# Performance work log

Hardware: AMD Instinct MI355X
Metric: run time of the kernel (lower is better)

The kernel has to match this reference:

```python
import jax, jax.numpy as jnp
import numpy as np

SPAN_W = 8      # fixed span width (tokens per span)
HID = 150       # Score hidden dim (hardcoded in source)


def _score_mlp(x, w1, b1, w2, b2, w3, b3):
    # Linear->ReLU->(Dropout=id)->Linear->ReLU->(Dropout=id)->Linear ; out dim 1
    h = jax.nn.relu(x @ w1 + b1)
    h = jax.nn.relu(h @ w2 + b2)
    return h @ w3 + b3


def _make_mlp_params(key, in_dim):
    ks = jax.random.split(key, 6)
    s1 = 1.0 / np.sqrt(in_dim)
    s2 = 1.0 / np.sqrt(HID)
    return (
        jax.random.uniform(ks[0], (in_dim, HID), jnp.float32, -s1, s1),
        jax.random.uniform(ks[1], (HID,), jnp.float32, -s1, s1),
        jax.random.uniform(ks[2], (HID, HID), jnp.float32, -s2, s2),
        jax.random.uniform(ks[3], (HID,), jnp.float32, -s2, s2),
        jax.random.uniform(ks[4], (HID, 1), jnp.float32, -s2, s2),
        jax.random.uniform(ks[5], (1,), jnp.float32, -s2, s2),
    )


def setup_inputs() -> dict:
    key = jax.random.key(0)
    k_emb, k_sp, k_a, k_m, k_p = jax.random.split(key, 5)
    E = 768
    B, T, S = 2, 2048, 96
    encoded_docs = jax.random.normal(k_emb, (B, T, E), jnp.float32)
    span_starts = jnp.sort(
        jax.random.randint(k_sp, (B, S), 0, 2040, dtype=jnp.int64), axis=-1)
    aw1, ab1, aw2, ab2, aw3, ab3 = _make_mlp_params(k_a, E)          # attn Score
    mw1, mb1, mw2, mb2, mw3, mb3 = _make_mlp_params(k_m, 3 * E)      # mention Score
    pw1, pb1, pw2, pb2, pw3, pb3 = _make_mlp_params(k_p, 9 * E)      # pair Score
    return {
        "encoded_docs": encoded_docs, "span_starts": span_starts,
        "aw1": aw1, "ab1": ab1, "aw2": aw2, "ab2": ab2, "aw3": aw3, "ab3": ab3,
        "mw1": mw1, "mb1": mb1, "mw2": mw2, "mb2": mb2, "mw3": mw3, "mb3": mb3,
        "pw1": pw1, "pb1": pb1, "pw2": pw2, "pb2": pb2, "pw3": pw3, "pb3": pb3,
    }


def reference(encoded_docs, span_starts,
              aw1, ab1, aw2, ab2, aw3, ab3,
              mw1, mb1, mw2, mb2, mw3, mb3,
              pw1, pb1, pw2, pb2, pw3, pb3):
    B, T, E = encoded_docs.shape
    S = span_starts.shape[1]

    # --- MentionScore ---
    attns = _score_mlp(encoded_docs, aw1, ab1, aw2, ab2, aw3, ab3)  # [B,T,1]
    starts = span_starts                                              # [B,S]
    ends = starts + (SPAN_W - 1)
    g_start = jnp.take_along_axis(encoded_docs, starts[:, :, None], axis=1)  # [B,S,E]
    g_end = jnp.take_along_axis(encoded_docs, ends[:, :, None], axis=1)      # [B,S,E]
    tok_idx = starts[:, :, None] + jnp.arange(SPAN_W, dtype=starts.dtype)     # [B,S,W]
    flat = tok_idx.reshape(B, S * SPAN_W)
    span_emb = jnp.take_along_axis(encoded_docs, flat[:, :, None], axis=1).reshape(B, S, SPAN_W, E)
    span_attn = jnp.take_along_axis(attns, flat[:, :, None], axis=1).reshape(B, S, SPAN_W, 1)
    g_attn = jnp.sum(span_emb * span_attn, axis=2)                    # [B,S,E]
    g_i = jnp.concatenate([g_start, g_end, g_attn], axis=-1)          # [B,S,3E]
    mention_scores = _score_mlp(g_i, mw1, mb1, mw2, mb2, mw3, mb3)    # [B,S,1]

    # --- PairwiseScore: all pairs (i=span_1, j=span_2) ---
    gi = jnp.broadcast_to(g_i[:, :, None, :], (B, S, S, 3 * E))
    gj = jnp.broadcast_to(g_i[:, None, :, :], (B, S, S, 3 * E))
    pair = jnp.concatenate([gi, gj, gi * gj], axis=-1)                # [B,S,S,9E]
    pair_scores = _score_mlp(pair, pw1, pb1, pw2, pb2, pw3, pb3)      # [B,S,S,1]
    ext = (mention_scores[:, :, None, :] + mention_scores[:, None, :, :] + pair_scores) / 3.0
    return jnp.clip(ext, 0.0, 1.0)
```

## Files before the change

kernel.cpp:

```cpp
#include <hip/hip_runtime.h>

#define EDIM   768
#define E3     2304
#define HIDD   150
#define TT     2048
#define SS     96
#define BB     2

typedef unsigned short u16;
using frag   = __attribute__((ext_vector_type(8))) short;
using f32x4v = __attribute__((ext_vector_type(4))) float;
using u16x8  = __attribute__((ext_vector_type(8))) unsigned short;

__device__ __forceinline__ u16 bf16rn(float f) {
    union { float f; unsigned u; } v; v.f = f;
    unsigned r = v.u + 0x7FFF + ((v.u >> 16) & 1);
    return (u16)(r >> 16);
}
__device__ __forceinline__ float bf16tof(u16 h) {
    union { unsigned u; float f; } v; v.u = ((unsigned)h) << 16;
    return v.f;
}
__device__ __forceinline__ void split2(float f, u16& hi, u16& lo) {
    hi = bf16rn(f); lo = bf16rn(f - bf16tof(hi));
}
__device__ __forceinline__ int swzoff(int row, int qd) {
    return row * 32 + (((qd + (row >> 1)) & 3) << 3);
}
__device__ __forceinline__ void async16(const void* g, void* l) {
    __builtin_amdgcn_global_load_lds(
        (const __attribute__((address_space(1))) void*)g,
        (__attribute__((address_space(3))) void*)l, 16, 0, 0);
}

__global__ __launch_bounds__(256) void k_prep_aw1(
    const float* __restrict__ aw1, u16* __restrict__ W_hi, u16* __restrict__ W_lo)
{
    const int k = blockIdx.x, t = threadIdx.x;
    if (t < 160) {
        float v = (t < HIDD) ? aw1[k * HIDD + t] : 0.f;
        u16 hi, lo; split2(v, hi, lo);
        W_hi[(long)t * EDIM + k] = hi;
        W_lo[(long)t * EDIM + k] = lo;
    }
}

__global__ __launch_bounds__(256) void k_fused1(
    const float* __restrict__ X, const int* __restrict__ spans,
    const u16* __restrict__ AW1t_hi, const u16* __restrict__ AW1t_lo,
    float* __restrict__ AH1,
    const float* __restrict__ pw1, const float* __restrict__ mw1,
    const float* __restrict__ aw2, const float* __restrict__ pw2,
    const float* __restrict__ mw2,
    u16* __restrict__ W12t_hi, u16* __restrict__ W12t_lo,
    u16* __restrict__ AW2t_hi, u16* __restrict__ AW2t_lo,
    u16* __restrict__ PW2t_hi, u16* __restrict__ PW2t_lo,
    u16* __restrict__ MW2t_hi, u16* __restrict__ MW2t_lo)
{
    __shared__ __align__(16) char smem[32768];
    const int id = blockIdx.x;
    const int t  = threadIdx.x;

    if (id < 288) {
        u16* As_hi = (u16*)smem;
        u16* As_lo = (u16*)(smem + 2560);
        u16* Bs_hi = (u16*)(smem + 5120);
        u16* Bs_lo = (u16*)(smem + 17920);

        const int lane = t & 63;
        const int m    = lane & 15;
        const int quad = lane >> 4;
        const int w    = t >> 6;
        const int mt   = (w & 1) * 16;
        const int nb   = (w >> 1) * 80;
        const int rb   = id % 48;
        const int ks   = id / 48;

        const int rr = t >> 3, q = t & 7;
        const int grow = rb * 32 + rr;
        const int bs = grow >> 3, sw = grow & 7;
        const int b  = bs / SS;
        const int tok = spans[bs] + sw;
        const float* arow = X + ((long)b * TT + tok) * EDIM;

        f32x4v acc[5];
        #pragma unroll
        for (int ht = 0; ht < 5; ++ht)
            #pragma unroll
            for (int r = 0; r < 4; ++r) acc[ht][r] = 0.f;

        for (int tt = 0; tt < 4; ++tt) {
            const int kk0 = ks * 128 + tt * 32;
            {
                const float4 xv = *(const float4*)&arow[kk0 + q * 4];
                ushort4 hv, lv;
                split2(xv.x, hv.x, lv.x); split2(xv.y, hv.y, lv.y);
                split2(xv.z, hv.z, lv.z); split2(xv.w, hv.w, lv.w);
                *(ushort4*)&As_hi[rr * 40 + q * 4] = hv;
                *(ushort4*)&As_lo[rr * 40 + q * 4] = lv;
            }
            #pragma unroll
            for (int it = 0; it < 3; ++it) {
                const int v = t + it * 256;
                if (v < 640) {
                    const int h = v >> 2, qq = v & 3;
                    *(uint4*)&Bs_hi[h * 40 + qq * 8] = *(const uint4*)&AW1t_hi[(long)h * EDIM + kk0 + qq * 8];
                    *(uint4*)&Bs_lo[h * 40 + qq * 8] = *(const uint4*)&AW1t_lo[(long)h * EDIM + kk0 + qq * 8];
                }
            }
            __syncthreads();
            const frag ah = *(const frag*)&As_hi[(mt + m) * 40 + quad * 8];
            const frag al = *(const frag*)&As_lo[(mt + m) * 40 + quad * 8];
            #pragma unroll
            for (int ht = 0; ht < 5; ++ht) {
                const frag bh = *(const frag*)&Bs_hi[(nb + ht * 16 + m) * 40 + quad * 8];
                const frag bl = *(const frag*)&Bs_lo[(nb + ht * 16 + m) * 40 + quad * 8];
                acc[ht] = __builtin_amdgcn_mfma_f32_16x16x32_bf16(al, bh, acc[ht], 0, 0, 0);
                acc[ht] = __builtin_amdgcn_mfma_f32_16x16x32_bf16(ah, bl, acc[ht], 0, 0, 0);
                acc[ht] = __builtin_amdgcn_mfma_f32_16x16x32_bf16(ah, bh, acc[ht], 0, 0, 0);
            }
            __syncthreads();
        }
        #pragma unroll
        for (int ht = 0; ht < 5; ++ht) {
            #pragma unroll
            for (int r = 0; r < 4; ++r) {
                const int row = rb * 32 + mt + quad * 4 + r;
                const int col = nb + ht * 16 + m;
                if (col < HIDD) atomicAdd(&AH1[row * 160 + col], acc[ht][r]);
            }
        }
    } else if (id < 1008) {
        float (*tile)[33] = (float(*)[33])smem;
        const int bi = id - 288;
        const int k0 = (bi % 36) * 64;
        const int n0 = (bi / 36) * 32;
        const int seg = n0 / 160;
        const int nloc0 = n0 - seg * 160;
        for (int idx = t; idx < 2048; idx += 256) {
            const int kk = idx >> 5, nn = idx & 31;
            const int nl = nloc0 + nn;
            const int k  = k0 + kk;
            float v = 0.f;
            if (nl < HIDD) {
                if (seg == 0)      v = pw1[(long)k * HIDD + nl];
                else if (seg == 1) v = pw1[(long)(E3 + k) * HIDD + nl];
                else if (seg == 2) v = mw1[(long)k * HIDD + nl];
                else               v = pw1[(long)(2 * E3 + k) * HIDD + nl];
            }
            tile[kk][nn] = v;
        }
        __syncthreads();
        for (int idx = t; idx < 2048; idx += 256) {
            const int nn = idx >> 6, kk = idx & 63;
            u16 hi, lo; split2(tile[kk][nn], hi, lo);
            W12t_hi[(long)(n0 + nn) * E3 + k0 + kk] = hi;
            W12t_lo[(long)(n0 + nn) * E3 + k0 + kk] = lo;
        }
    } else {
        const int r = id - 1008;
        const int k = r % 160;
        const int which = r / 160;
        const float* src = (which == 0) ? aw2 : (which == 1) ? pw2 : mw2;
        u16* dh = (which == 0) ? AW2t_hi : (which == 1) ? PW2t_hi : MW2t_hi;
        u16* dl = (which == 0) ? AW2t_lo : (which == 1) ? PW2t_lo : MW2t_lo;
        if (t < 160) {
            float v = (t < HIDD && k < HIDD) ? src[k * HIDD + t] : 0.f;
            u16 hi, lo; split2(v, hi, lo);
            dh[t * 160 + k] = hi;
            dl[t * 160 + k] = lo;
        }
    }
}

__global__ __launch_bounds__(256) void k_attn2(
    const float* __restrict__ AH1,
    const u16* __restrict__ AW2t_hi, const u16* __restrict__ AW2t_lo,
    const float* __restrict__ ab1, const float* __restrict__ ab2,
    const float* __restrict__ aw3, const float* __restrict__ ab3,
    float* __restrict__ attn_g)
{
    __shared__ __align__(16) u16 As_hi[32 * 40];
    __shared__ __align__(16) u16 As_lo[32 * 40];
    __shared__ __align__(16) u16 Bs_hi[160 * 40];
    __shared__ __align__(16) u16 Bs_lo[160 * 40];
    __shared__ float h1s[32 * 160];
    __shared__ float red[32];

    const int t    = threadIdx.x;
    const int lane = t & 63;
    const int m    = lane & 15;
    const int quad = lane >> 4;
    const int w    = t >> 6;
    const int mt   = (w & 1) * 16;
    const int nb   = (w >> 1) * 80;

    for (int u = t; u < 1280; u += 256) {
        const int row = u / 40, c4 = u - (u / 40) * 40;
        const int c0 = c4 * 4;
        const float4 v = *(const float4*)&AH1[(blockIdx.x * 32 + row) * 160 + c0];
        h1s[row * 160 + c0 + 0] = (c0 + 0 < HIDD) ? fmaxf(v.x + ab1[c0 + 0], 0.f) : 0.f;
        h1s[row * 160 + c0 + 1] = (c0 + 1 < HIDD) ? fmaxf(v.y + ab1[c0 + 1], 0.f) : 0.f;
        h1s[row * 160 + c0 + 2] = (c0 + 2 < HIDD) ? fmaxf(v.z + ab1[c0 + 2], 0.f) : 0.f;
        h1s[row * 160 + c0 + 3] = (c0 + 3 < HIDD) ? fmaxf(v.w + ab1[c0 + 3], 0.f) : 0.f;
    }
    if (t < 32) red[t] = 0.f;
    __syncthreads();

    const int rr = t >> 3, q = t & 7;
    f32x4v acc2[5];
    #pragma unroll
    for (int ht = 0; ht < 5; ++ht)
        #pragma unroll
        for (int r = 0; r < 4; ++r) acc2[ht][r] = 0.f;

    for (int kk = 0; kk < 5; ++kk) {
        {
            const float4 xv = *(const float4*)&h1s[rr * 160 + kk * 32 + q * 4];
            ushort4 hv, lv;
            split2(xv.x, hv.x, lv.x); split2(xv.y, hv.y, lv.y);
            split2(xv.z, hv.z, lv.z); split2(xv.w, hv.w, lv.w);
            *(ushort4*)&As_hi[rr * 40 + q * 4] = hv;
            *(ushort4*)&As_lo[rr * 40 + q * 4] = lv;
        }
        #pragma unroll
        for (int it = 0; it < 3; ++it) {
            const int v = t + it * 256;
            if (v < 640) {
                const int h = v >> 2, qq = v & 3;
                *(uint4*)&Bs_hi[h * 40 + qq * 8] = *(const uint4*)&AW2t_hi[h * 160 + kk * 32 + qq * 8];
                *(uint4*)&Bs_lo[h * 40 + qq * 8] = *(const uint4*)&AW2t_lo[h * 160 + kk * 32 + qq * 8];
            }
        }
        __syncthreads();
        const frag ah = *(const frag*)&As_hi[(mt + m) * 40 + quad * 8];
        const frag al = *(const frag*)&As_lo[(mt + m) * 40 + quad * 8];
        #pragma unroll
        for (int ht = 0; ht < 5; ++ht) {
            const frag bh = *(const frag*)&Bs_hi[(nb + ht * 16 + m) * 40 + quad * 8];
            const frag bl = *(const frag*)&Bs_lo[(nb + ht * 16 + m) * 40 + quad * 8];
            acc2[ht] = __builtin_amdgcn_mfma_f32_16x16x32_bf16(al, bh, acc2[ht], 0, 0, 0);
            acc2[ht] = __builtin_amdgcn_mfma_f32_16x16x32_bf16(ah, bl, acc2[ht], 0, 0, 0);
            acc2[ht] = __builtin_amdgcn_mfma_f32_16x16x32_bf16(ah, bh, acc2[ht], 0, 0, 0);
        }
        __syncthreads();
    }

    float s[4] = {0.f, 0.f, 0.f, 0.f};
    #pragma unroll
    for (int ht = 0; ht < 5; ++ht) {
        const int col = nb + ht * 16 + m;
        if (col < HIDD) {
            const float w3 = aw3[col];
            #pragma unroll
            for (int r = 0; r < 4; ++r)
                s[r] += fmaxf(acc2[ht][r] + ab2[col], 0.f) * w3;
        }
    }
    #pragma unroll
    for (int r = 0; r < 4; ++r) {
        for (int off = 8; off > 0; off >>= 1) s[r] += __shfl_down(s[r], off, 16);
    }
    if (m == 0) {
        #pragma unroll
        for (int r = 0; r < 4; ++r) atomicAdd(&red[mt + quad * 4 + r], s[r]);
    }
    __syncthreads();
    if (t < 32) attn_g[blockIdx.x * 32 + t] = red[t] + ab3[0];
}

__global__ __launch_bounds__(256) void k_span_g(
    const float* __restrict__ X, const int* __restrict__ spans,
    const float* __restrict__ attn_g, float* __restrict__ G_ws,
    u16* __restrict__ Gs_hi, u16* __restrict__ Gs_lo)
{
    __shared__ float a8[8];
    const int t  = threadIdx.x;
    const int bs = blockIdx.x;
    const int b  = bs / SS;
    const int start = spans[bs];
    const float* xb = X + ((long)b * TT + start) * EDIM;
    float* Gp = G_ws + (long)bs * E3;
    u16* Gh = Gs_hi + (long)bs * E3;
    u16* Gl = Gs_lo + (long)bs * E3;
    if (t < 8) a8[t] = attn_g[bs * 8 + t];
    __syncthreads();

    for (int e = t; e < EDIM; e += 256) {
        const float gs = xb[e];
        const float ge = xb[7 * EDIM + e];
        float ga = 0.f;
        #pragma unroll
        for (int w = 0; w < 8; ++w) ga += xb[w * EDIM + e] * a8[w];
        Gp[e] = gs; Gp[EDIM + e] = ge; Gp[2 * EDIM + e] = ga;
        u16 hi, lo;
        split2(gs, hi, lo); Gh[e] = hi;            Gl[e] = lo;
        split2(ge, hi, lo); Gh[EDIM + e] = hi;     Gl[EDIM + e] = lo;
        split2(ga, hi, lo); Gh[2 * EDIM + e] = hi; Gl[2 * EDIM + e] = lo;
    }
}

__global__ __launch_bounds__(256) void k_heavy(
    const float* __restrict__ G_ws,
    const u16* __restrict__ Gs_hi, const u16* __restrict__ Gs_lo,
    const u16* __restrict__ W12t_hi, const u16* __restrict__ W12t_lo,
    const u16* __restrict__ PCt_hi, const u16* __restrict__ PCt_lo,
    float* __restrict__ H1parts, float* __restrict__ UVM)
{
    __shared__ __align__(16) char smem[48128];
    const int id = blockIdx.x;
    const int t  = threadIdx.x;
    const int lane = t & 63;
    const int m    = lane & 15;
    const int quad = lane >> 4;
    const int w    = t >> 6;

    if (id < 576) {
        float* gis  = (float*)smem;
        float* gjst = (float*)(smem + 3072);
        u16* As_hi  = (u16*)(smem + 15360);
        u16* As_lo  = (u16*)(smem + 21504);
        u16* Bs_hi  = (u16*)(smem + 27648);
        u16* Bs_lo  = (u16*)(smem + 37888);

        const int ks = id % 3;
        const int i  = (id / 3) % SS;
        const int b  = id / 288;
        const int ksbase = ks * 768;
        const int jt0 = i >> 4;
        const int ntiles = 6 - jt0;
        const int j0 = jt0 * 16;
        const int R  = 96 - j0;
        const int nI = R >> 3;

        const int hb   = (w & 1) * 80;
        const int apar = w >> 1;
        const int Bl_h = lane >> 2;
        const int Bl_c = lane & 3;
        const int gj_r = lane >> 3;
        const int gj_c = lane & 7;

        const float* Gi = G_ws + (long)(b * SS + i) * E3 + ksbase;
        for (int e = t; e < 768; e += 256) gis[e] = Gi[e];

        f32x4v acc[3][5];
        #pragma unroll
        for (int jt = 0; jt < 3; ++jt)
            #pragma unroll
            for (int ht = 0; ht < 5; ++ht)
                #pragma unroll
                for (int r = 0; r < 4; ++r) acc[jt][ht][r] = 0.f;

        for (int tt = 0; tt < 24; ++tt) {
            const int kk0 = ksbase + tt * 32;
            for (int q2 = w; q2 < 10; q2 += 4) {
                const int h  = q2 * 16 + Bl_h;
                const int qd = (Bl_c - (h >> 1)) & 3;
                const long so = (long)h * E3 + kk0 + qd * 8;
                async16(&PCt_hi[so], &Bs_hi[q2 * 512]);
                async16(&PCt_lo[so], &Bs_lo[q2 * 512]);
            }
            for (int g2 = w; g2 < nI; g2 += 4) {
                const int row = j0 + g2 * 8 + gj_r;
                async16(&G_ws[(long)(b * SS + row) * E3 + kk0 + gj_c * 4],
                        &gjst[g2 * 256]);
            }
            __syncthreads();

            for (int u = t; u < R * 4; u += 256) {
                const int rr = u >> 2, qd = u & 3;
                const float4 g0 = *(const float4*)&gjst[rr * 32 + qd * 8];
                const float4 g1 = *(const float4*)&gjst[rr * 32 + qd * 8 + 4];
                const int kl = tt * 32 + qd * 8;
                u16x8 hv, lv; u16 h, l;
                split2(g0.x * gis[kl + 0], h, l); hv[0] = h; lv[0] = l;
                split2(g0.y * gis[kl + 1], h, l); hv[1] = h; lv[1] = l;
                split2(g0.z * gis[kl + 2], h, l); hv[2] = h; lv[2] = l;
                split2(g0.w * gis[kl + 3], h, l); hv[3] = h; lv[3] = l;
                split2(g1.x * gis[kl + 4], h, l); hv[4] = h; lv[4] = l;
                split2(g1.y * gis[kl + 5], h, l); hv[5] = h; lv[5] = l;
                split2(g1.z * gis[kl + 6], h, l); hv[6] = h; lv[6] = l;
                split2(g1.w * gis[kl + 7], h, l); hv[7] = h; lv[7] = l;
                const int o = swzoff(rr, qd);
                *(u16x8*)&As_hi[o] = hv;
                *(u16x8*)&As_lo[o] = lv;
            }
            __syncthreads();

            frag ah[3], al[3];
            #pragma unroll
            for (int u = 0; u < 3; ++u) {
                const int a = apar + 2 * u;
                if (a < ntiles) {
                    const int o = swzoff(a * 16 + m, quad);
                    ah[u] = *(const frag*)&As_hi[o];
                    al[u] = *(const frag*)&As_lo[o];
                }
            }
            #pragma unroll
            for (int ht = 0; ht < 5; ++ht) {
                const int o = swzoff(hb + ht * 16 + m, quad);
                const frag bh = *(const frag*)&Bs_hi[o];
                const frag bl = *(const frag*)&Bs_lo[o];
                #pragma unroll
                for (int u = 0; u < 3; ++u) {
                    if (apar + 2 * u < ntiles) {
                        acc[u][ht] = __builtin_amdgcn_mfma_f32_16x16x32_bf16(al[u], bh, acc[u][ht], 0, 0, 0);
                        acc[u][ht] = __builtin_amdgcn_mfma_f32_16x16x32_bf16(ah[u], bl, acc[u][ht], 0, 0, 0);
                        acc[u][ht] = __builtin_amdgcn_mfma_f32_16x16x32_bf16(ah[u], bh, acc[u][ht], 0, 0, 0);
                    }
                }
            }
            __syncthreads();
        }

        float* dst = H1parts + (long)ks * ((long)BB * SS * SS * 160);
        #pragma unroll
        for (int u = 0; u < 3; ++u) {
            const int a = apar + 2 * u;
            if (a < ntiles) {
                #pragma unroll
                for (int ht = 0; ht < 5; ++ht) {
                    #pragma unroll
                    for (int r = 0; r < 4; ++r) {
                        const int j = (jt0 + a) * 16 + quad * 4 + r;
                        const int h = hb + ht * 16 + m;
                        dst[((long)(b * SS + i) * SS + j) * 160 + h] = acc[u][ht][r];
                    }
                }
            }
        }
    } else {
        u16* As_hi = (u16*)smem;
        u16* As_lo = (u16*)(smem + 5120);
        u16* Bs_hi = (u16*)(smem + 10240);
        u16* Bs_lo = (u16*)(smem + 23040);

        const int u0 = id - 576;
        const int mb = u0 % 3;
        const int nb = (u0 / 3) % 3;
        const int kz = u0 / 9;
        const int mhalf = (w & 1) * 32;
        const int nbase = (w >> 1) * 80;
        const int arr = t >> 2, aq = t & 3;

        f32x4v acc[2][5];
        #pragma unroll
        for (int i = 0; i < 2; ++i)
            #pragma unroll
            for (int j = 0; j < 5; ++j)
                #pragma unroll
                for (int r = 0; r < 4; ++r) acc[i][j][r] = 0.f;

        for (int tt = 0; tt < 6; ++tt) {
            const int kk0 = kz * 192 + tt * 32;
            *(uint4*)&As_hi[arr * 40 + aq * 8] = *(const uint4*)&Gs_hi[(long)(mb * 64 + arr) * E3 + kk0 + aq * 8];
            *(uint4*)&As_lo[arr * 40 + aq * 8] = *(const uint4*)&Gs_lo[(long)(mb * 64 + arr) * E3 + kk0 + aq * 8];
            #pragma unroll
            for (int it = 0; it < 3; ++it) {
                const int v = t + it * 256;
                if (v < 640) {
                    const int h = v >> 2, qq = v & 3;
                    *(uint4*)&Bs_hi[h * 40 + qq * 8] = *(const uint4*)&W12t_hi[(long)(nb * 160 + h) * E3 + kk0 + qq * 8];
                    *(uint4*)&Bs_lo[h * 40 + qq * 8] = *(const uint4*)&W12t_lo[(long)(nb * 160 + h) * E3 + kk0 + qq * 8];
                }
            }
            __syncthreads();
            frag ah[2], al[2];
            #pragma unroll
            for (int mt = 0; mt < 2; ++mt) {
                ah[mt] = *(const frag*)&As_hi[(mhalf + mt * 16 + m) * 40 + quad * 8];
                al[mt] = *(const frag*)&As_lo[(mhalf + mt * 16 + m) * 40 + quad * 8];
            }
            #pragma unroll
            for (int ht = 0; ht < 5; ++ht) {
                const frag bh = *(const frag*)&Bs_hi[(nbase + ht * 16 + m) * 40 + quad * 8];
                const frag bl = *(const frag*)&Bs_lo[(nbase + ht * 16 + m) * 40 + quad * 8];
                #pragma unroll
                for (int mt = 0; mt < 2; ++mt) {
                    acc[mt][ht] = __builtin_amdgcn_mfma_f32_16x16x32_bf16(al[mt], bh, acc[mt][ht], 0, 0, 0);
                    acc[mt][ht] = __builtin_amdgcn_mfma_f32_16x16x32_bf16(ah[mt], bl, acc[mt][ht], 0, 0, 0);
                    acc[mt][ht] = __builtin_amdgcn_mfma_f32_16x16x32_bf16(ah[mt], bh, acc[mt][ht], 0, 0, 0);
                }
            }
            __syncthreads();
        }
        float* dst = UVM + (long)nb * (192 * 160);
        #pragma unroll
        for (int mt = 0; mt < 2; ++mt) {
            #pragma unroll
            for (int ht = 0; ht < 5; ++ht) {
                #pragma unroll
                for (int r = 0; r < 4; ++r) {
                    const int row = mb * 64 + mhalf + mt * 16 + quad * 4 + r;
                    const int c   = nbase + ht * 16 + m;
                    atomicAdd(&dst[row * 160 + c], acc[mt][ht][r]);
                }
            }
        }
    }
}

__global__ __launch_bounds__(256) void k_pair2(
    const float* __restrict__ H1parts,
    const float* __restrict__ U_ws, const float* __restrict__ V_ws,
    const float* __restrict__ pb1, const float* __restrict__ m_ws,
    const u16* __restrict__ PW2t_hi, const u16* __restrict__ PW2t_lo,
    const float* __restrict__ pb2, const float* __restrict__ pw3,
    const float* __restrict__ pb3,
    float* __restrict__ out)
{
    __shared__ __align__(16) u16 As_hi[32 * 168];
    __shared__ __align__(16) u16 As_lo[32 * 168];
    __shared__ __align__(16) u16 Bs_hi[160 * 40];
    __shared__ __align__(16) u16 Bs_lo[160 * 40];
    __shared__ float uv[160];
    __shared__ float red[32];

    const long partsz = (long)BB * SS * SS * 160;
    const int t  = threadIdx.x;
    const int js = blockIdx.x;
    const int bi = blockIdx.y;
    const int b  = bi / SS;
    const int ii = bi - b * SS;
    const int jb0 = js * 32;

    if (t < 160) uv[t] = U_ws[bi * 160 + t] + ((t < HIDD) ? pb1[t] : 0.f);
    if (t < 32) red[t] = 0.f;
    __syncthreads();

    for (int u = t; u < 32 * 40; u += 256) {
        const int jl = u / 40, hq = u - (u / 40) * 40;
        const int j  = jb0 + jl;
        const int h0 = hq * 4;
        const int mn = ii < j ? ii : j;
        const int mx = ii < j ? j : ii;
        const long idx = (((long)b * SS + mn) * SS + mx) * 160 + h0;
        const float4 vv = *(const float4*)&V_ws[(b * SS + j) * 160 + h0];
        const float4 a0 = *(const float4*)&H1parts[idx];
        const float4 a1 = *(const float4*)&H1parts[partsz + idx];
        const float4 a2 = *(const float4*)&H1parts[2 * partsz + idx];
        const float p0 = fmaxf(a0.x + a1.x + a2.x + vv.x + uv[h0 + 0], 0.f);
        const float p1 = fmaxf(a0.y + a1.y + a2.y + vv.y + uv[h0 + 1], 0.f);
        const float p2 = fmaxf(a0.z + a1.z + a2.z + vv.z + uv[h0 + 2], 0.f);
        const float p3 = fmaxf(a0.w + a1.w + a2.w + vv.w + uv[h0 + 3], 0.f);
        ushort4 hv, lv;
        split2(p0, hv.x, lv.x); split2(p1, hv.y, lv.y);
        split2(p2, hv.z, lv.z); split2(p3, hv.w, lv.w);
        *(ushort4*)&As_hi[jl * 168 + h0] = hv;
        *(ushort4*)&As_lo[jl * 168 + h0] = lv;
    }
    __syncthreads();

    const int lane = t & 63;
    const int m    = lane & 15;
    const int quad = lane >> 4;
    const int w    = t >> 6;
    const int jt   = w >> 1;
    const int nbs  = (w & 1) * 80;

    f32x4v acc[5];
    #pragma unroll
    for (int ht = 0; ht < 5; ++ht)
        #pragma unroll
        for (int r = 0; r < 4; ++r) acc[ht][r] = 0.f;

    for (int kk = 0; kk < 5; ++kk) {
        #pragma unroll
        for (int it = 0; it < 3; ++it) {
            const int v = t + it * 256;
            if (v < 640) {
                const int n = v >> 2, qq = v & 3;
                *(uint4*)&Bs_hi[n * 40 + qq * 8] = *(const uint4*)&PW2t_hi[n * 160 + kk * 32 + qq * 8];
                *(uint4*)&Bs_lo[n * 40 + qq * 8] = *(const uint4*)&PW2t_lo[n * 160 + kk * 32 + qq * 8];
            }
        }
        __syncthreads();
        const frag ah = *(const frag*)&As_hi[(jt * 16 + m) * 168 + kk * 32 + quad * 8];
        const frag al = *(const frag*)&As_lo[(jt * 16 + m) * 168 + kk * 32 + quad * 8];
        #pragma unroll
        for (int ht = 0; ht < 5; ++ht) {
            const frag bh = *(const frag*)&Bs_hi[(nbs + ht * 16 + m) * 40 + quad * 8];
            const frag bl = *(const frag*)&Bs_lo[(nbs + ht * 16 + m) * 40 + quad * 8];
            acc[ht] = __builtin_amdgcn_mfma_f32_16x16x32_bf16(al, bh, acc[ht], 0, 0, 0);
            acc[ht] = __builtin_amdgcn_mfma_f32_16x16x32_bf16(ah, bl, acc[ht], 0, 0, 0);
            acc[ht] = __builtin_amdgcn_mfma_f32_16x16x32_bf16(ah, bh, acc[ht], 0, 0, 0);
        }
        __syncthreads();
    }

    float s[4] = {0.f, 0.f, 0.f, 0.f};
    #pragma unroll
    for (int ht = 0; ht < 5; ++ht) {
        const int col = nbs + ht * 16 + m;
        if (col < HIDD) {
            const float w3 = pw3[col];
            const float b2 = pb2[col];
            #pragma unroll
            for (int r = 0; r < 4; ++r)
                s[r] += fmaxf(acc[ht][r] + b2, 0.f) * w3;
        }
    }
    #pragma unroll
    for (int r = 0; r < 4; ++r)
        for (int off = 8; off > 0; off >>= 1)
            s[r] += __shfl_down(s[r], off, 16);
    if (m == 0) {
        #pragma unroll
        for (int r = 0; r < 4; ++r)
            atomicAdd(&red[jt * 16 + quad * 4 + r], s[r]);
    }
    __syncthreads();

    if (t < 32) {
        const int j = jb0 + t;
        const float sc = red[t] + pb3[0];
        const float v = (m_ws[bi] + m_ws[b * SS + j] + sc) * (1.f / 3.f);
        out[(long)bi * SS + j] = fminf(fmaxf(v, 0.f), 1.f);
    }
}

extern "C" void kernel_launch(void* const* d_in, const int* in_sizes, int n_in,
                              void* d_out, int out_size, void* d_ws, size_t ws_size,
                              hipStream_t stream)
{
    const float* X     = (const float*)d_in[0];
    const int*   spans = (const int*)  d_in[1];
    const float* aw1 = (const float*)d_in[2];
    const float* ab1 = (const float*)d_in[3];
    const float* aw2 = (const float*)d_in[4];
    const float* ab2 = (const float*)d_in[5];
    const float* aw3 = (const float*)d_in[6];
    const float* ab3 = (const float*)d_in[7];
    const float* mw1 = (const float*)d_in[8];
    const float* mb1 = (const float*)d_in[9];
    const float* mw2 = (const float*)d_in[10];
    const float* mb2 = (const float*)d_in[11];
    const float* mw3 = (const float*)d_in[12];
    const float* mb3 = (const float*)d_in[13];
    const float* pw1 = (const float*)d_in[14];
    const float* pb1 = (const float*)d_in[15];
    const float* pw2 = (const float*)d_in[16];
    const float* pb2 = (const float*)d_in[17];
    const float* pw3 = (const float*)d_in[18];
    const float* pb3 = (const float*)d_in[19];
    float* out = (float*)d_out;

    char* p = (char*)d_ws;
    float* attn_g  = (float*)p;  p += 6144;
    float* G_ws    = (float*)p;  p += (long)442368 * 4;
    u16*   Gs_hi   = (u16*)p;    p += (long)442368 * 2;
    u16*   Gs_lo   = (u16*)p;    p += (long)442368 * 2;
    float* UVM     = (float*)p;  p += (long)3 * 192 * 160 * 4;
    float* AH1     = (float*)p;  p += (long)1536 * 160 * 4;
    float* m_ws    = (float*)p;  p += 1024;
    u16*   W12t_hi = (u16*)p;    p += (long)640 * E3 * 2;
    u16*   W12t_lo = (u16*)p;    p += (long)640 * E3 * 2;
    u16*   AW1t_hi = (u16*)p;    p += (long)160 * EDIM * 2;
    u16*   AW1t_lo = (u16*)p;    p += (long)160 * EDIM * 2;
    u16*   AW2t_hi = (u16*)p;    p += 160 * 160 * 2;
    u16*   AW2t_lo = (u16*)p;    p += 160 * 160 * 2;
    u16*   PW2t_hi = (u16*)p;    p += 160 * 160 * 2;
    u16*   PW2t_lo = (u16*)p;    p += 160 * 160 * 2;
    u16*   MW2t_hi = (u16*)p;    p += 160 * 160 * 2;
    u16*   MW2t_lo = (u16*)p;    p += 160 * 160 * 2;
    float* H1parts = (float*)p;

    float* U_ws = UVM;
    float* V_ws = UVM + 192 * 160;
    float* M_ws = UVM + 2 * 192 * 160;
    const u16* PCt_hi = W12t_hi + (long)480 * E3;
    const u16* PCt_lo = W12t_lo + (long)480 * E3;

    hipMemsetAsync(UVM, 0, ((size_t)3 * 192 * 160 + (size_t)1536 * 160) * sizeof(float), stream);

    k_prep_aw1<<<dim3(EDIM), 256, 0, stream>>>(aw1, AW1t_hi, AW1t_lo);

    k_fused1<<<dim3(1488), 256, 0, stream>>>(X, spans, AW1t_hi, AW1t_lo, AH1,
                                             pw1, mw1, aw2, pw2, mw2,
                                             W12t_hi, W12t_lo, AW2t_hi, AW2t_lo,
                                             PW2t_hi, PW2t_lo, MW2t_hi, MW2t_lo);

    k_attn2<<<dim3(48), 256, 0, stream>>>(AH1, AW2t_hi, AW2t_lo, ab1, ab2, aw3, ab3, attn_g);
    k_span_g<<<dim3(BB * SS), 256, 0, stream>>>(X, spans, attn_g, G_ws, Gs_hi, Gs_lo);

    k_heavy<<<dim3(684), 256, 0, stream>>>(G_ws, Gs_hi, Gs_lo, W12t_hi, W12t_lo,
                                           PCt_hi, PCt_lo, H1parts, UVM);

    k_attn2<<<dim3(6), 256, 0, stream>>>(M_ws, MW2t_hi, MW2t_lo, mb1, mb2, mw3, mb3, m_ws);

    k_pair2<<<dim3(3, BB * SS), 256, 0, stream>>>(
        H1parts, U_ws, V_ws, pb1, m_ws, PW2t_hi, PW2t_lo, pb2, pw3, pb3, out);
}
```

Baseline: 213.9 us.

## Merge small dependent kernels using in-kernel atomic flags and split-K partial buffers

Fuses the attention-MLP second layer with span embedding gathering, and the mention-score MLP with the pairwise final stage, into single launches. Inside each merged launch, consumer blocks spin on a global atomic counter until the producer blocks signal completion. The first-layer attention GEMM now writes split-K partials to separate buffers instead of using atomicAdd, and the consumer sums them, which also shrinks the memset. This removes launch gaps and atomic contention, but spin-waiting assumes the producer blocks are scheduled before or alongside the waiters, and the merged kernels use more shared memory.

```diff
diff --git a/kernel.cpp b/kernel.cpp
--- a/kernel.cpp
+++ b/kernel.cpp
@@ -31,6 +31,17 @@
     __builtin_amdgcn_global_load_lds(
         (const __attribute__((address_space(1))) void*)g,
         (__attribute__((address_space(3))) void*)l, 16, 0, 0);
+}
+__device__ __forceinline__ void signal_done(int* flag) {
+    __syncthreads();
+    if (threadIdx.x == 0)
+        __hip_atomic_fetch_add(flag, 1, __ATOMIC_RELEASE, __HIP_MEMORY_SCOPE_AGENT);
+}
+__device__ __forceinline__ void wait_for(int* flag, int target) {
+    if (threadIdx.x == 0) {
+        while (__hip_atomic_load(flag, __ATOMIC_ACQUIRE, __HIP_MEMORY_SCOPE_AGENT) < target) {}
+    }
+    __syncthreads();
 }
 
 __global__ __launch_bounds__(256) void k_prep_aw1(
@@ -48,7 +59,7 @@
 __global__ __launch_bounds__(256) void k_fused1(
     const float* __restrict__ X, const int* __restrict__ spans,
     const u16* __restrict__ AW1t_hi, const u16* __restrict__ AW1t_lo,
-    float* __restrict__ AH1,
+    float* __restrict__ AH1parts,
     const float* __restrict__ pw1, const float* __restrict__ mw1,
     const float* __restrict__ aw2, const float* __restrict__ pw2,
     const float* __restrict__ mw2,
@@ -121,13 +132,14 @@
             }
             __syncthreads();
         }
+        float* dst = AH1parts + (long)ks * (1536 * 160);
         #pragma unroll
         for (int ht = 0; ht < 5; ++ht) {
             #pragma unroll
             for (int r = 0; r < 4; ++r) {
                 const int row = rb * 32 + mt + quad * 4 + r;
                 const int col = nb + ht * 16 + m;
-                if (col < HIDD) atomicAdd(&AH1[row * 160 + col], acc[ht][r]);
+                dst[row * 160 + col] = acc[ht][r];
             }
         }
     } else if (id < 1008) {
@@ -173,130 +185,143 @@
     }
 }
 
-__global__ __launch_bounds__(256) void k_attn2(
-    const float* __restrict__ AH1,
+__global__ __launch_bounds__(256) void k_attn2span(
+    const float* __restrict__ X, const int* __restrict__ spans,
+    const float* __restrict__ AH1parts,
     const u16* __restrict__ AW2t_hi, const u16* __restrict__ AW2t_lo,
     const float* __restrict__ ab1, const float* __restrict__ ab2,
     const float* __restrict__ aw3, const float* __restrict__ ab3,
-    float* __restrict__ attn_g)
+    float* __restrict__ attn_g, float* __restrict__ G_ws,
+    u16* __restrict__ Gs_hi, u16* __restrict__ Gs_lo,
+    int* __restrict__ flag)
 {
-    __shared__ __align__(16) u16 As_hi[32 * 40];
-    __shared__ __align__(16) u16 As_lo[32 * 40];
-    __shared__ __align__(16) u16 Bs_hi[160 * 40];
-    __shared__ __align__(16) u16 Bs_lo[160 * 40];
-    __shared__ float h1s[32 * 160];
-    __shared__ float red[32];
-
-    const int t    = threadIdx.x;
-    const int lane = t & 63;
-    const int m    = lane & 15;
-    const int quad = lane >> 4;
-    const int w    = t >> 6;
-    const int mt   = (w & 1) * 16;
-    const int nb   = (w >> 1) * 80;
-
-    for (int u = t; u < 1280; u += 256) {
-        const int row = u / 40, c4 = u - (u / 40) * 40;
-        const int c0 = c4 * 4;
-        const float4 v = *(const float4*)&AH1[(blockIdx.x * 32 + row) * 160 + c0];
-        h1s[row * 160 + c0 + 0] = (c0 + 0 < HIDD) ? fmaxf(v.x + ab1[c0 + 0], 0.f) : 0.f;
-        h1s[row * 160 + c0 + 1] = (c0 + 1 < HIDD) ? fmaxf(v.y + ab1[c0 + 1], 0.f) : 0.f;
-        h1s[row * 160 + c0 + 2] = (c0 + 2 < HIDD) ? fmaxf(v.z + ab1[c0 + 2], 0.f) : 0.f;
-        h1s[row * 160 + c0 + 3] = (c0 + 3 < HIDD) ? fmaxf(v.w + ab1[c0 + 3], 0.f) : 0.f;
-    }
-    if (t < 32) red[t] = 0.f;
-    __syncthreads();
-
-    const int rr = t >> 3, q = t & 7;
-    f32x4v acc2[5];
-    #pragma unroll
-    for (int ht = 0; ht < 5; ++ht)
-        #pragma unroll
-        for (int r = 0; r < 4; ++r) acc2[ht][r] = 0.f;
-
-    for (int kk = 0; kk < 5; ++kk) {
-        {
-            const float4 xv = *(const float4*)&h1s[rr * 160 + kk * 32 + q * 4];
-            ushort4 hv, lv;
-            split2(xv.x, hv.x, lv.x); split2(xv.y, hv.y, lv.y);
-            split2(xv.z, hv.z, lv.z); split2(xv.w, hv.w, lv.w);
-            *(ushort4*)&As_hi[rr * 40 + q * 4] = hv;
-            *(ushort4*)&As_lo[rr * 40 + q * 4] = lv;
-        }
-        #pragma unroll
-        for (int it = 0; it < 3; ++it) {
-            const int v = t + it * 256;
-            if (v < 640) {
-                const int h = v >> 2, qq = v & 3;
-                *(uint4*)&Bs_hi[h * 40 + qq * 8] = *(const uint4*)&AW2t_hi[h * 160 + kk * 32 + qq * 8];
-                *(uint4*)&Bs_lo[h * 40 + qq * 8] = *(const uint4*)&AW2t_lo[h * 160 + kk * 32 + qq * 8];
-            }
-        }
+    __shared__ __align__(16) char smem[51328];
+    const int id = blockIdx.x;
+    const int t  = threadIdx.x;
+
+    if (id < 48) {
+        u16* As_hi = (u16*)smem;
+        u16* As_lo = (u16*)(smem + 2560);
+        u16* Bs_hi = (u16*)(smem + 5120);
+        u16* Bs_lo = (u16*)(smem + 17920);
+        float* h1s = (float*)(smem + 30720);
+        float* red = (float*)(smem + 51200);
+
+        const int lane = t & 63;
+        const int m    = lane & 15;
+        const int quad = lane >> 4;
+        const int w    = t >> 6;
+        const int mt   = (w & 1) * 16;
+        const int nb   = (w >> 1) * 80;
+
+        for (int u = t; u < 1280; u += 256) {
+            const int row = u / 40, c4 = u - (u / 40) * 40;
+            const int c0 = c4 * 4;
+            const long off = (long)(id * 32 + row) * 160 + c0;
+            float4 s = *(const float4*)&AH1parts[off];
+            #pragma unroll
+            for (int pp = 1; pp < 6; ++pp) {
+                const float4 v = *(const float4*)&AH1parts[(long)pp * 245760 + off];
+                s.x += v.x; s.y += v.y; s.z += v.z; s.w += v.w;
+            }
+            h1s[row * 160 + c0 + 0] = (c0 + 0 < HIDD) ? fmaxf(s.x + ab1[c0 + 0], 0.f) : 0.f;
+            h1s[row * 160 + c0 + 1] = (c0 + 1 < HIDD) ? fmaxf(s.y + ab1[c0 + 1], 0.f) : 0.f;
+            h1s[row * 160 + c0 + 2] = (c0 + 2 < HIDD) ? fmaxf(s.z + ab1[c0 + 2], 0.f) : 0.f;
+            h1s[row * 160 + c0 + 3] = (c0 + 3 < HIDD) ? fmaxf(s.w + ab1[c0 + 3], 0.f) : 0.f;
+        }
+        if (t < 32) red[t] = 0.f;
         __syncthreads();
-        const frag ah = *(const frag*)&As_hi[(mt + m) * 40 + quad * 8];
-        const frag al = *(const frag*)&As_lo[(mt + m) * 40 + quad * 8];
+
+        const int rr = t >> 3, q = t & 7;
+        f32x4v acc2[5];
+        #pragma unroll
+        for (int ht = 0; ht < 5; ++ht)
+            #pragma unroll
+            for (int r = 0; r < 4; ++r) acc2[ht][r] = 0.f;
+
+        for (int kk = 0; kk < 5; ++kk) {
+            {
+                const float4 xv = *(const float4*)&h1s[rr * 160 + kk * 32 + q * 4];
+                ushort4 hv, lv;
+                split2(xv.x, hv.x, lv.x); split2(xv.y, hv.y, lv.y);
+                split2(xv.z, hv.z, lv.z); split2(xv.w, hv.w, lv.w);
+                *(ushort4*)&As_hi[rr * 40 + q * 4] = hv;
+                *(ushort4*)&As_lo[rr * 40 + q * 4] = lv;
+            }
+            #pragma unroll
+            for (int it = 0; it < 3; ++it) {
+                const int v = t + it * 256;
+                if (v < 640) {
+                    const int h = v >> 2, qq = v & 3;
+                    *(uint4*)&Bs_hi[h * 40 + qq * 8] = *(const uint4*)&AW2t_hi[h * 160 + kk * 32 + qq * 8];
+                    *(uint4*)&Bs_lo[h * 40 + qq * 8] = *(const uint4*)&AW2t_lo[h * 160 + kk * 32 + qq * 8];
+                }
+            }
+            __syncthreads();
+            const frag ah = *(const frag*)&As_hi[(mt + m) * 40 + quad * 8];
+            const frag al = *(const frag*)&As_lo[(mt + m) * 40 + quad * 8];
+            #pragma unroll
+            for (int ht = 0; ht < 5; ++ht) {
+                const frag bh = *(const frag*)&Bs_hi[(nb + ht * 16 + m) * 40 + quad * 8];
+                const frag bl = *(const frag*)&Bs_lo[(nb + ht * 16 + m) * 40 + quad * 8];
+                acc2[ht] = __builtin_amdgcn_mfma_f32_16x16x32_bf16(al, bh, acc2[ht], 0, 0, 0);
+                acc2[ht] = __builtin_amdgcn_mfma_f32_16x16x32_bf16(ah, bl, acc2[ht], 0, 0, 0);
+                acc2[ht] = __builtin_amdgcn_mfma_f32_16x16x32_bf16(ah, bh, acc2[ht], 0, 0, 0);
+            }
+            __syncthreads();
+        }
+
+        float s[4] = {0.f, 0.f, 0.f, 0.f};
         #pragma unroll
         for (int ht = 0; ht < 5; ++ht) {
-            const frag bh = *(const frag*)&Bs_hi[(nb + ht * 16 + m) * 40 + quad * 8];
-            const frag bl = *(const frag*)&Bs_lo[(nb + ht * 16 + m) * 40 + quad * 8];
-            acc2[ht] = __builtin_amdgcn_mfma_f32_16x16x32_bf16(al, bh, acc2[ht], 0, 0, 0);
-            acc2[ht] = __builtin_amdgcn_mfma_f32_16x16x32_bf16(ah, bl, acc2[ht], 0, 0, 0);
-            acc2[ht] = __builtin_amdgcn_mfma_f32_16x16x32_bf16(ah, bh, acc2[ht], 0, 0, 0);
+            const int col = nb + ht * 16 + m;
+            if (col < HIDD) {
+                const float w3 = aw3[col];
+                #pragma unroll
+                for (int r = 0; r < 4; ++r)
+                    s[r] += fmaxf(acc2[ht][r] + ab2[col], 0.f) * w3;
+            }
+        }
+        #pragma unroll
+        for (int r = 0; r < 4; ++r) {
+            for (int off = 8; off > 0; off >>= 1) s[r] += __shfl_down(s[r], off, 16);
+        }
+        if (m == 0) {
+            #pragma unroll
+            for (int r = 0; r < 4; ++r) atomicAdd(&red[mt + quad * 4 + r], s[r]);
         }
         __syncthreads();
-    }
-
-    float s[4] = {0.f, 0.f, 0.f, 0.f};
-    #pragma unroll
-    for (int ht = 0; ht < 5; ++ht) {
-        const int col = nb + ht * 16 + m;
-        if (col < HIDD) {
-            const float w3 = aw3[col];
-            #pragma unroll
-            for (int r = 0; r < 4; ++r)
-                s[r] += fmaxf(acc2[ht][r] + ab2[col], 0.f) * w3;
-        }
-    }
-    #pragma unroll
-    for (int r = 0; r < 4; ++r) {
-        for (int off = 8; off > 0; off >>= 1) s[r] += __shfl_down(s[r], off, 16);
-    }
-    if (m == 0) {
-        #pragma unroll
-        for (int r = 0; r < 4; ++r) atomicAdd(&red[mt + quad * 4 + r], s[r]);
-    }
-    __syncthreads();
-    if (t < 32) attn_g[blockIdx.x * 32 + t] = red[t] + ab3[0];
-}
-
-__global__ __launch_bounds__(256) void k_span_g(
-    const float* __restrict__ X, const int* __restrict__ spans,
-    const float* __restrict__ attn_g, float* __restrict__ G_ws,
-    u16* __restrict__ Gs_hi, u16* __restrict__ Gs_lo)
-{
-    __shared__ float a8[8];
-    const int t  = threadIdx.x;
-    const int bs = blockIdx.x;
-    const int b  = bs / SS;
-    const int start = spans[bs];
-    const float* xb = X + ((long)b * TT + start) * EDIM;
-    float* Gp = G_ws + (long)bs * E3;
-    u16* Gh = Gs_hi + (long)bs * E3;
-    u16* Gl = Gs_lo + (long)bs * E3;
-    if (t < 8) a8[t] = attn_g[bs * 8 + t];
-    __syncthreads();
-
-    for (int e = t; e < EDIM; e += 256) {
-        const float gs = xb[e];
-        const float ge = xb[7 * EDIM + e];
-        float ga = 0.f;
-        #pragma unroll
-        for (int w = 0; w < 8; ++w) ga += xb[w * EDIM + e] * a8[w];
-        Gp[e] = gs; Gp[EDIM + e] = ge; Gp[2 * EDIM + e] = ga;
-        u16 hi, lo;
-        split2(gs, hi, lo); Gh[e] = hi;            Gl[e] = lo;
-        split2(ge, hi, lo); Gh[EDIM + e] = hi;     Gl[EDIM + e] = lo;
-        split2(ga, hi, lo); Gh[2 * EDIM + e] = hi; Gl[2 * EDIM + e] = lo;
+        if (t < 32) attn_g[id * 32 + t] = red[t] + ab3[0];
+        signal_done(flag);
+    } else {
+        float* a8 = (float*)smem;
+        const int bs = id - 48;
+        const int b  = bs / SS;
+        const int start = spans[bs];
+        const float* xb = X + ((long)b * TT + start) * EDIM;
+        float* Gp = G_ws + (long)bs * E3;
+        u16* Gh = Gs_hi + (long)bs * E3;
+        u16* Gl = Gs_lo + (long)bs * E3;
+
+        for (int e = t; e < EDIM; e += 256) {
+            const float gs = xb[e];
+            const float ge = xb[7 * EDIM + e];
+            Gp[e] = gs; Gp[EDIM + e] = ge;
+            u16 hi, lo;
+            split2(gs, hi, lo); Gh[e] = hi;        Gl[e] = lo;
+            split2(ge, hi, lo); Gh[EDIM + e] = hi; Gl[EDIM + e] = lo;
+        }
+        wait_for(flag, 48);
+        if (t < 8) a8[t] = attn_g[bs * 8 + t];
+        __syncthreads();
+        for (int e = t; e < EDIM; e += 256) {
+            float ga = 0.f;
+            #pragma unroll
+            for (int w = 0; w < 8; ++w) ga += xb[w * EDIM + e] * a8[w];
+            Gp[2 * EDIM + e] = ga;
+            u16 hi, lo; split2(ga, hi, lo);
+            Gh[2 * EDIM + e] = hi; Gl[2 * EDIM + e] = lo;
+        }
     }
 }
 
@@ -501,122 +526,218 @@
     }
 }
 
-__global__ __launch_bounds__(256) void k_pair2(
+__global__ __launch_bounds__(256) void k_final(
     const float* __restrict__ H1parts,
     const float* __restrict__ U_ws, const float* __restrict__ V_ws,
-    const float* __restrict__ pb1, const float* __restrict__ m_ws,
+    const float* __restrict__ M_ws,
+    const float* __restrict__ pb1, float* __restrict__ m_ws,
     const u16* __restrict__ PW2t_hi, const u16* __restrict__ PW2t_lo,
+    const u16* __restrict__ MW2t_hi, const u16* __restrict__ MW2t_lo,
+    const float* __restrict__ mb1, const float* __restrict__ mb2,
+    const float* __restrict__ mw3, const float* __restrict__ mb3,
     const float* __restrict__ pb2, const float* __restrict__ pw3,
     const float* __restrict__ pb3,
+    int* __restrict__ flag,
     float* __restrict__ out)
 {
-    __shared__ __align__(16) u16 As_hi[32 * 168];
-    __shared__ __align__(16) u16 As_lo[32 * 168];
-    __shared__ __align__(16) u16 Bs_hi[160 * 40];
-    __shared__ __align__(16) u16 Bs_lo[160 * 40];
-    __shared__ float uv[160];
-    __shared__ float red[32];
-
-    const long partsz = (long)BB * SS * SS * 160;
+    __shared__ __align__(16) char smem[51328];
+    const int id = blockIdx.x;
     const int t  = threadIdx.x;
-    const int js = blockIdx.x;
-    const int bi = blockIdx.y;
-    const int b  = bi / SS;
-    const int ii = bi - b * SS;
-    const int jb0 = js * 32;
-
-    if (t < 160) uv[t] = U_ws[bi * 160 + t] + ((t < HIDD) ? pb1[t] : 0.f);
-    if (t < 32) red[t] = 0.f;
-    __syncthreads();
-
-    for (int u = t; u < 32 * 40; u += 256) {
-        const int jl = u / 40, hq = u - (u / 40) * 40;
-        const int j  = jb0 + jl;
-        const int h0 = hq * 4;
-        const int mn = ii < j ? ii : j;
-        const int mx = ii < j ? j : ii;
-        const long idx = (((long)b * SS + mn) * SS + mx) * 160 + h0;
-        const float4 vv = *(const float4*)&V_ws[(b * SS + j) * 160 + h0];
-        const float4 a0 = *(const float4*)&H1parts[idx];
-        const float4 a1 = *(const float4*)&H1parts[partsz + idx];
-        const float4 a2 = *(const float4*)&H1parts[2 * partsz + idx];
-        const float p0 = fmaxf(a0.x + a1.x + a2.x + vv.x + uv[h0 + 0], 0.f);
-        const float p1 = fmaxf(a0.y + a1.y + a2.y + vv.y + uv[h0 + 1], 0.f);
-        const float p2 = fmaxf(a0.z + a1.z + a2.z + vv.z + uv[h0 + 2], 0.f);
-        const float p3 = fmaxf(a0.w + a1.w + a2.w + vv.w + uv[h0 + 3], 0.f);
-        ushort4 hv, lv;
-        split2(p0, hv.x, lv.x); split2(p1, hv.y, lv.y);
-        split2(p2, hv.z, lv.z); split2(p3, hv.w, lv.w);
-        *(ushort4*)&As_hi[jl * 168 + h0] = hv;
-        *(ushort4*)&As_lo[jl * 168 + h0] = lv;
-    }
-    __syncthreads();
-
     const int lane = t & 63;
     const int m    = lane & 15;
     const int quad = lane >> 4;
     const int w    = t >> 6;
-    const int jt   = w >> 1;
-    const int nbs  = (w & 1) * 80;
-
-    f32x4v acc[5];
-    #pragma unroll
-    for (int ht = 0; ht < 5; ++ht)
-        #pragma unroll
-        for (int r = 0; r < 4; ++r) acc[ht][r] = 0.f;
-
-    for (int kk = 0; kk < 5; ++kk) {
-        #pragma unroll
-        for (int it = 0; it < 3; ++it) {
-            const int v = t + it * 256;
-            if (v < 640) {
-                const int n = v >> 2, qq = v & 3;
-                *(uint4*)&Bs_hi[n * 40 + qq * 8] = *(const uint4*)&PW2t_hi[n * 160 + kk * 32 + qq * 8];
-                *(uint4*)&Bs_lo[n * 40 + qq * 8] = *(const uint4*)&PW2t_lo[n * 160 + kk * 32 + qq * 8];
-            }
-        }
+
+    if (id < 6) {
+        u16* As_hi = (u16*)smem;
+        u16* As_lo = (u16*)(smem + 2560);
+        u16* Bs_hi = (u16*)(smem + 5120);
+        u16* Bs_lo = (u16*)(smem + 17920);
+        float* h1s = (float*)(smem + 30720);
+        float* red = (float*)(smem + 51200);
+
+        const int mt = (w & 1) * 16;
+        const int nb = (w >> 1) * 80;
+
+        for (int u = t; u < 1280; u += 256) {
+            const int row = u / 40, c4 = u - (u / 40) * 40;
+            const int c0 = c4 * 4;
+            const float4 v = *(const float4*)&M_ws[(id * 32 + row) * 160 + c0];
+            h1s[row * 160 + c0 + 0] = (c0 + 0 < HIDD) ? fmaxf(v.x + mb1[c0 + 0], 0.f) : 0.f;
+            h1s[row * 160 + c0 + 1] = (c0 + 1 < HIDD) ? fmaxf(v.y + mb1[c0 + 1], 0.f) : 0.f;
+            h1s[row * 160 + c0 + 2] = (c0 + 2 < HIDD) ? fmaxf(v.z + mb1[c0 + 2], 0.f) : 0.f;
+            h1s[row * 160 + c0 + 3] = (c0 + 3 < HIDD) ? fmaxf(v.w + mb1[c0 + 3], 0.f) : 0.f;
+        }
+        if (t < 32) red[t] = 0.f;
         __syncthreads();
-        const frag ah = *(const frag*)&As_hi[(jt * 16 + m) * 168 + kk * 32 + quad * 8];
-        const frag al = *(const frag*)&As_lo[(jt * 16 + m) * 168 + kk * 32 + quad * 8];
+
+        const int rr = t >> 3, q = t & 7;
+        f32x4v acc2[5];
+        #pragma unroll
+        for (int ht = 0; ht < 5; ++ht)
+            #pragma unroll
+            for (int r = 0; r < 4; ++r) acc2[ht][r] = 0.f;
+
+        for (int kk = 0; kk < 5; ++kk) {
+            {
+                const float4 xv = *(const float4*)&h1s[rr * 160 + kk * 32 + q * 4];
+                ushort4 hv, lv;
+                split2(xv.x, hv.x, lv.x); split2(xv.y, hv.y, lv.y);
+                split2(xv.z, hv.z, lv.z); split2(xv.w, hv.w, lv.w);
+                *(ushort4*)&As_hi[rr * 40 + q * 4] = hv;
+                *(ushort4*)&As_lo[rr * 40 + q * 4] = lv;
+            }
+            #pragma unroll
+            for (int it = 0; it < 3; ++it) {
+                const int v = t + it * 256;
+                if (v < 640) {
+                    const int h = v >> 2, qq = v & 3;
+                    *(uint4*)&Bs_hi[h * 40 + qq * 8] = *(const uint4*)&MW2t_hi[h * 160 + kk * 32 + qq * 8];
+                    *(uint4*)&Bs_lo[h * 40 + qq * 8] = *(const uint4*)&MW2t_lo[h * 160 + kk * 32 + qq * 8];
+                }
+            }
+            __syncthreads();
+            const frag ah = *(const frag*)&As_hi[(mt + m) * 40 + quad * 8];
+            const frag al = *(const frag*)&As_lo[(mt + m) * 40 + quad * 8];
+            #pragma unroll
+            for (int ht = 0; ht < 5; ++ht) {
+                const frag bh = *(const frag*)&Bs_hi[(nb + ht * 16 + m) * 40 + quad * 8];
+                const frag bl = *(const frag*)&Bs_lo[(nb + ht * 16 + m) * 40 + quad * 8];
+                acc2[ht] = __builtin_amdgcn_mfma_f32_16x16x32_bf16(al, bh, acc2[ht], 0, 0, 0);
+                acc2[ht] = __builtin_amdgcn_mfma_f32_16x16x32_bf16(ah, bl, acc2[ht], 0, 0, 0);
+                acc2[ht] = __builtin_amdgcn_mfma_f32_16x16x32_bf16(ah, bh, acc2[ht], 0, 0, 0);
+            }
+            __syncthreads();
+        }
+
+        float s[4] = {0.f, 0.f, 0.f, 0.f};
         #pragma unroll
         for (int ht = 0; ht < 5; ++ht) {
-            const frag bh = *(const frag*)&Bs_hi[(nbs + ht * 16 + m) * 40 + quad * 8];
-            const frag bl = *(const frag*)&Bs_lo[(nbs + ht * 16 + m) * 40 + quad * 8];
-            acc[ht] = __builtin_amdgcn_mfma_f32_16x16x32_bf16(al, bh, acc[ht], 0, 0, 0);
-            acc[ht] = __builtin_amdgcn_mfma_f32_16x16x32_bf16(ah, bl, acc[ht], 0, 0, 0);
-            acc[ht] = __builtin_amdgcn_mfma_f32_16x16x32_bf16(ah, bh, acc[ht], 0, 0, 0);
+            const int col = nb + ht * 16 + m;
+            if (col < HIDD) {
+                const float w3 = mw3[col];
+                #pragma unroll
+                for (int r = 0; r < 4; ++r)
+                    s[r] += fmaxf(acc2[ht][r] + mb2[col], 0.f) * w3;
+            }
+        }
+        #pragma unroll
+        for (int r = 0; r < 4; ++r) {
+            for (int off = 8; off > 0; off >>= 1) s[r] += __shfl_down(s[r], off, 16);
+        }
+        if (m == 0) {
+            #pragma unroll
+            for (int r = 0; r < 4; ++r) atomicAdd(&red[mt + quad * 4 + r], s[r]);
         }
         __syncthreads();
-    }
-
-    float s[4] = {0.f, 0.f, 0.f, 0.f};
-    #pragma unroll
-    for (int ht = 0; ht < 5; ++ht) {
-        const int col = nbs + ht * 16 + m;
-        if (col < HIDD) {
-            const float w3 = pw3[col];
-            const float b2 = pb2[col];
+        if (t < 32) m_ws[id * 32 + t] = red[t] + mb3[0];
+        signal_done(flag);
+    } else {
+        u16* As_hi = (u16*)smem;
+        u16* As_lo = (u16*)(smem + 10752);
+        u16* Bs_hi = (u16*)(smem + 21504);
+        u16* Bs_lo = (u16*)(smem + 34304);
+        float* uv  = (float*)(smem + 47104);
+        float* red = (float*)(smem + 47744);
+
+        const long partsz = (long)BB * SS * SS * 160;
+        const int pid = id - 6;
+        const int js  = pid % 3;
+        const int bi  = pid / 3;
+        const int b   = bi / SS;
+        const int ii  = bi - b * SS;
+        const int jb0 = js * 32;
+
+        if (t < 160) uv[t] = U_ws[bi * 160 + t] + ((t < HIDD) ? pb1[t] : 0.f);
+        if (t < 32) red[t] = 0.f;
+        __syncthreads();
+
+        for (int u = t; u < 32 * 40; u += 256) {
+            const int jl = u / 40, hq = u - (u / 40) * 40;
+            const int j  = jb0 + jl;
+            const int h0 = hq * 4;
+            const int mn = ii < j ? ii : j;
+            const int mx = ii < j ? j : ii;
+            const long idx = (((long)b * SS + mn) * SS + mx) * 160 + h0;
+            const float4 vv = *(const float4*)&V_ws[(b * SS + j) * 160 + h0];
+            const float4 a0 = *(const float4*)&H1parts[idx];
+            const float4 a1 = *(const float4*)&H1parts[partsz + idx];
+            const float4 a2 = *(const float4*)&H1parts[2 * partsz + idx];
+            const float p0 = fmaxf(a0.x + a1.x + a2.x + vv.x + uv[h0 + 0], 0.f);
+            const float p1 = fmaxf(a0.y + a1.y + a2.y + vv.y + uv[h0 + 1], 0.f);
+            const float p2 = fmaxf(a0.z + a1.z + a2.z + vv.z + uv[h0 + 2], 0.f);
+            const float p3 = fmaxf(a0.w + a1.w + a2.w + vv.w + uv[h0 + 3], 0.f);
+            ushort4 hv, lv;
+            split2(p0, hv.x, lv.x); split2(p1, hv.y, lv.y);
+            split2(p2, hv.z, lv.z); split2(p3, hv.w, lv.w);
+            *(ushort4*)&As_hi[jl * 168 + h0] = hv;
+            *(ushort4*)&As_lo[jl * 168 + h0] = lv;
+        }
+        __syncthreads();
+
+        const int jt  = w >> 1;
+        const int nbs = (w & 1) * 80;
+
+        f32x4v acc[5];
+        #pragma unroll
+        for (int ht = 0; ht < 5; ++ht)
+            #pragma unroll
+            for (int r = 0; r < 4; ++r) acc[ht][r] = 0.f;
+
+        for (int kk = 0; kk < 5; ++kk) {
+            #pragma unroll
+            for (int it = 0; it < 3; ++it) {
+                const int v = t + it * 256;
+                if (v < 640) {
+                    const int n = v >> 2, qq = v & 3;
+                    *(uint4*)&Bs_hi[n * 40 + qq * 8] = *(const uint4*)&PW2t_hi[n * 160 + kk * 32 + qq * 8];
+                    *(uint4*)&Bs_lo[n * 40 + qq * 8] = *(const uint4*)&PW2t_lo[n * 160 + kk * 32 + qq * 8];
+                }
+            }
+            __syncthreads();
+            const frag ah = *(const frag*)&As_hi[(jt * 16 + m) * 168 + kk * 32 + quad * 8];
+            const frag al = *(const frag*)&As_lo[(jt * 16 + m) * 168 + kk * 32 + quad * 8];
+            #pragma unroll
+            for (int ht = 0; ht < 5; ++ht) {
+                const frag bh = *(const frag*)&Bs_hi[(nbs + ht * 16 + m) * 40 + quad * 8];
+                const frag bl = *(const frag*)&Bs_lo[(nbs + ht * 16 + m) * 40 + quad * 8];
+                acc[ht] = __builtin_amdgcn_mfma_f32_16x16x32_bf16(al, bh, acc[ht], 0, 0, 0);
+                acc[ht] = __builtin_amdgcn_mfma_f32_16x16x32_bf16(ah, bl, acc[ht], 0, 0, 0);
+                acc[ht] = __builtin_amdgcn_mfma_f32_16x16x32_bf16(ah, bh, acc[ht], 0, 0, 0);
+            }
+            __syncthreads();
+        }
+
+        float s[4] = {0.f, 0.f, 0.f, 0.f};
+        #pragma unroll
+        for (int ht = 0; ht < 5; ++ht) {
+            const int col = nbs + ht * 16 + m;
+            if (col < HIDD) {
+                const float w3 = pw3[col];
+                const float b2 = pb2[col];
+                #pragma unroll
+                for (int r = 0; r < 4; ++r)
+                    s[r] += fmaxf(acc[ht][r] + b2, 0.f) * w3;
+            }
+        }
+        #pragma unroll
+        for (int r = 0; r < 4; ++r)
+            for (int off = 8; off > 0; off >>= 1)
+                s[r] += __shfl_down(s[r], off, 16);
+        if (m == 0) {
             #pragma unroll
             for (int r = 0; r < 4; ++r)
-                s[r] += fmaxf(acc[ht][r] + b2, 0.f) * w3;
-        }
-    }
-    #pragma unroll
-    for (int r = 0; r < 4; ++r)
-        for (int off = 8; off > 0; off >>= 1)
-            s[r] += __shfl_down(s[r], off, 16);
-    if (m == 0) {
-        #pragma unroll
-        for (int r = 0; r < 4; ++r)
-            atomicAdd(&red[jt * 16 + quad * 4 + r], s[r]);
-    }
-    __syncthreads();
-
-    if (t < 32) {
-        const int j = jb0 + t;
-        const float sc = red[t] + pb3[0];
-        const float v = (m_ws[bi] + m_ws[b * SS + j] + sc) * (1.f / 3.f);
-        out[(long)bi * SS + j] = fminf(fmaxf(v, 0.f), 1.f);
+                atomicAdd(&red[jt * 16 + quad * 4 + r], s[r]);
+        }
+        __syncthreads();
+
+        wait_for(flag, 6);
+        if (t < 32) {
+            const int j = jb0 + t;
+            const float sc = red[t] + pb3[0];
+            const float v = (m_ws[bi] + m_ws[b * SS + j] + sc) * (1.f / 3.f);
+            out[(long)bi * SS + j] = fminf(fmaxf(v, 0.f), 1.f);
+        }
     }
 }
 
@@ -652,7 +773,8 @@
     u16*   Gs_hi   = (u16*)p;    p += (long)442368 * 2;
     u16*   Gs_lo   = (u16*)p;    p += (long)442368 * 2;
     float* UVM     = (float*)p;  p += (long)3 * 192 * 160 * 4;
-    float* AH1     = (float*)p;  p += (long)1536 * 160 * 4;
+    int*   flags   = (int*)p;    p += 256;
+    float* AH1parts= (float*)p;  p += (long)6 * 1536 * 160 * 4;
     float* m_ws    = (float*)p;  p += 1024;
     u16*   W12t_hi = (u16*)p;    p += (long)640 * E3 * 2;
     u16*   W12t_lo = (u16*)p;    p += (long)640 * E3 * 2;
@@ -672,23 +794,24 @@
     const u16* PCt_hi = W12t_hi + (long)480 * E3;
     const u16* PCt_lo = W12t_lo + (long)480 * E3;
 
-    hipMemsetAsync(UVM, 0, ((size_t)3 * 192 * 160 + (size_t)1536 * 160) * sizeof(float), stream);
+    hipMemsetAsync(UVM, 0, (size_t)3 * 192 * 160 * sizeof(float) + 256, stream);
 
     k_prep_aw1<<<dim3(EDIM), 256, 0, stream>>>(aw1, AW1t_hi, AW1t_lo);
 
-    k_fused1<<<dim3(1488), 256, 0, stream>>>(X, spans, AW1t_hi, AW1t_lo, AH1,
+    k_fused1<<<dim3(1488), 256, 0, stream>>>(X, spans, AW1t_hi, AW1t_lo, AH1parts,
                                              pw1, mw1, aw2, pw2, mw2,
                                              W12t_hi, W12t_lo, AW2t_hi, AW2t_lo,
                                              PW2t_hi, PW2t_lo, MW2t_hi, MW2t_lo);
 
-    k_attn2<<<dim3(48), 256, 0, stream>>>(AH1, AW2t_hi, AW2t_lo, ab1, ab2, aw3, ab3, attn_g);
-    k_span_g<<<dim3(BB * SS), 256, 0, stream>>>(X, spans, attn_g, G_ws, Gs_hi, Gs_lo);
+    k_attn2span<<<dim3(240), 256, 0, stream>>>(X, spans, AH1parts,
+                                               AW2t_hi, AW2t_lo, ab1, ab2, aw3, ab3,
+                                               attn_g, G_ws, Gs_hi, Gs_lo, &flags[0]);
 
     k_heavy<<<dim3(684), 256, 0, stream>>>(G_ws, Gs_hi, Gs_lo, W12t_hi, W12t_lo,
                                            PCt_hi, PCt_lo, H1parts, UVM);
 
-    k_attn2<<<dim3(6), 256, 0, stream>>>(M_ws, MW2t_hi, MW2t_lo, mb1, mb2, mw3, mb3, m_ws);
-
-    k_pair2<<<dim3(3, BB * SS), 256, 0, stream>>>(
-        H1parts, U_ws, V_ws, pb1, m_ws, PW2t_hi, PW2t_lo, pb2, pw3, pb3, out);
-}
+    k_final<<<dim3(582), 256, 0, stream>>>(H1parts, U_ws, V_ws, M_ws,
+                                           pb1, m_ws, PW2t_hi, PW2t_lo,
+                                           MW2t_hi, MW2t_lo, mb1, mb2, mw3, mb3,
+                                           pb2, pw3, pb3, &flags[1], out);
+}
```

Result: slower. 297.8 us (+39.2%).
